# Performance work log

Hardware: AMD Instinct MI355X
Metric: run time of the kernel (lower is better)

Reference implementation:

```python
import jax, jax.numpy as jnp
import numpy as np

N, E, D, H, C = 50000, 800000, 128, 4, 32  # nodes, edges, in/out dim, heads, head dim
NEG_SLOPE = 0.2
LN_EPS = 1e-5
NORM_EPS = 1e-12


def setup_inputs() -> dict:
    key = jax.random.key(0)
    ks = jax.random.split(key, 10)
    s = 1.0 / np.sqrt(D)
    return {
        "x": jax.random.normal(ks[0], (N, D), dtype=jnp.float32),
        "edge_index": jax.random.randint(ks[1], (2, E), 0, N, dtype=jnp.int64),
        "gamma": 1.0 + 0.1 * jax.random.normal(ks[2], (D,), dtype=jnp.float32),
        "beta": 0.1 * jax.random.normal(ks[3], (D,), dtype=jnp.float32),
        "W_l": jax.random.normal(ks[4], (D, H * C), dtype=jnp.float32) * s,
        "b_l": jnp.zeros((H * C,), dtype=jnp.float32),
        "W_r": jax.random.normal(ks[5], (D, H * C), dtype=jnp.float32) * s,
        "b_r": jnp.zeros((H * C,), dtype=jnp.float32),
        "att": jax.random.normal(ks[6], (H, C), dtype=jnp.float32) * s,
        "bias": jnp.zeros((H * C,), dtype=jnp.float32),
        "scale": jnp.array(1.0, dtype=jnp.float32),
    }


def reference(x, edge_index, gamma, beta, W_l, b_l, W_r, b_r, att, bias, scale):
    n = x.shape[0]
    # Pre-activation: LayerNorm -> ReLU (dropout=0 in eval)
    mu = jnp.mean(x, axis=-1, keepdims=True)
    var = jnp.mean(jnp.square(x - mu), axis=-1, keepdims=True)
    h = jax.nn.relu((x - mu) / jnp.sqrt(var + LN_EPS) * gamma + beta)

    # GATv2Conv (PyG defaults: add_self_loops=True, negative_slope=0.2)
    loops = jnp.arange(n, dtype=edge_index.dtype)
    src = jnp.concatenate([edge_index[0], loops])  # message source j
    dst = jnp.concatenate([edge_index[1], loops])  # message target i

    xl = (h @ W_l + b_l).reshape(n, H, C)
    xr = (h @ W_r + b_r).reshape(n, H, C)

    # per-edge GATv2 score: a^T LeakyReLU(xl[j] + xr[i])  -> [E2, H]
    feat = jax.nn.leaky_relu(xl[src] + xr[dst], NEG_SLOPE)
    e = jnp.einsum('ehc,hc->eh', feat, att)

    # segment softmax over incoming edges of each target node
    m = jax.ops.segment_max(e, dst, num_segments=n)
    p = jnp.exp(e - m[dst])
    denom = jax.ops.segment_sum(p, dst, num_segments=n)
    alpha = p / denom[dst]  # [E2, H]

    # scatter-aggregate weighted source features
    msg = alpha[:, :, None] * xl[src]  # [E2, H, C]
    out = jax.ops.segment_sum(msg, dst, num_segments=n).reshape(n, H * C) + bias

    # MsgNorm: normalize(msg) * ||h||_2 * scale
    out_norm = jnp.sqrt(jnp.sum(jnp.square(out), axis=-1, keepdims=True))
    msg_n = out / jnp.maximum(out_norm, NORM_EPS)
    h_norm = jnp.sqrt(jnp.sum(jnp.square(h), axis=-1, keepdims=True))
    gat_out = msg_n * h_norm * scale

    # residual (projection is None since in_channels == out_channels)
    return x + gat_out
```

## Files before the change

### kernel.cpp

```cpp
#include <hip/hip_runtime.h>
#include <hip/hip_bf16.h>
#include <math.h>

#define N_NODES 50000
#define N_EDGES 800000
#define E2 (N_EDGES + N_NODES)
#define D 128

#define NB_LN 12500
#define NB_W 128

#define BSHIFT 8
#define NBUCK 196
#define SCHUNK 4096
#define NB_SC ((E2 + SCHUNK - 1) / SCHUNK)
#define NB_GEMM (((N_NODES + 127) / 128) * 2)

typedef short short8 __attribute__((ext_vector_type(8)));
typedef float f32x4 __attribute__((ext_vector_type(4)));
typedef _Float16 h16x2 __attribute__((ext_vector_type(2)));
typedef _Float16 h16x8 __attribute__((ext_vector_type(8)));

__device__ __forceinline__ float waveReduceSum(float v) {
#pragma unroll
  for (int off = 32; off >= 1; off >>= 1) v += __shfl_xor(v, off);
  return v;
}

__global__ void __launch_bounds__(256) k_pre(
    const float* __restrict__ x, const float* __restrict__ gamma,
    const float* __restrict__ beta, const float* __restrict__ Wl,
    const float* __restrict__ Wr, const int* __restrict__ ei,
    __hip_bfloat16* __restrict__ hb, float* __restrict__ hnorm,
    __hip_bfloat16* __restrict__ Wt, int* __restrict__ bcnt) {
  const int b = blockIdx.x;
  if (b < NB_LN) {
    int wid = threadIdx.x >> 6;
    int lane = threadIdx.x & 63;
    int i = b * 4 + wid;
    const float2 xv = *(const float2*)&x[(size_t)i * D + lane * 2];
    float s = waveReduceSum(xv.x + xv.y);
    float mean = s * (1.0f / D);
    float d0 = xv.x - mean, d1 = xv.y - mean;
    float vs = waveReduceSum(d0 * d0 + d1 * d1);
    float rstd = rsqrtf(vs * (1.0f / D) + 1e-5f);
    const float2 g = *(const float2*)&gamma[lane * 2];
    const float2 bb = *(const float2*)&beta[lane * 2];
    float h0 = fmaxf(d0 * rstd * g.x + bb.x, 0.0f);
    float h1 = fmaxf(d1 * rstd * g.y + bb.y, 0.0f);
    __hip_bfloat162 hv;
    hv.x = __float2bfloat16(h0);
    hv.y = __float2bfloat16(h1);
    *(__hip_bfloat162*)&hb[(size_t)i * D + lane * 2] = hv;
    float ns = waveReduceSum(h0 * h0 + h1 * h1);
    if (lane == 0) hnorm[i] = sqrtf(ns);
  } else if (b < NB_LN + NB_W) {
    int local = b - NB_LN;
    int n = local * 2 + (threadIdx.x >> 7);
    int k = threadIdx.x & 127;
    float v = (n < D) ? Wl[(size_t)k * D + n] : Wr[(size_t)k * D + (n - D)];
    Wt[n * D + k] = __float2bfloat16(v);
  } else {
    __shared__ int c[256];
    const int t = threadIdx.x;
    c[t] = 0;
    __syncthreads();
    const int s0 = (b - NB_LN - NB_W) * SCHUNK;
#pragma unroll
    for (int k = 0; k < 16; ++k) {
      int e = s0 + t + k * 256;
      if (e < E2) {
        int dst = (e < N_EDGES) ? ei[N_EDGES + e] : (e - N_EDGES);
        atomicAdd(&c[dst >> BSHIFT], 1);
      }
    }
    __syncthreads();
    if (c[t]) atomicAdd(&bcnt[t], c[t]);
  }
}

__global__ void __launch_bounds__(256) k_bscatter(const int* __restrict__ ei,
                                                  const int* __restrict__ bcnt,
                                                  int* __restrict__ cnt0,
                                                  int2* __restrict__ bucketed) {
  __shared__ int c[256], base[256], sd[256];
  const int t = threadIdx.x;
  const int own = (t < NBUCK) ? bcnt[t] : 0;
  sd[t] = own;
  c[t] = 0;
  __syncthreads();
  for (int off = 1; off < 256; off <<= 1) {
    int u = 0;
    if (t >= off) u = sd[t - off];
    __syncthreads();
    if (t >= off) sd[t] += u;
    __syncthreads();
  }
  const int boffL = sd[t] - own;
  const int s0 = blockIdx.x * SCHUNK;
#pragma unroll
  for (int k = 0; k < 16; ++k) {
    int e = s0 + t + k * 256;
    if (e < E2) {
      int dst = (e < N_EDGES) ? ei[N_EDGES + e] : (e - N_EDGES);
      atomicAdd(&c[dst >> BSHIFT], 1);
    }
  }
  __syncthreads();
  if (t < NBUCK) {
    base[t] = c[t] ? (boffL + atomicAdd(&cnt0[t], c[t])) : 0;
    c[t] = 0;
  }
  __syncthreads();
#pragma unroll
  for (int k = 0; k < 16; ++k) {
    int e = s0 + t + k * 256;
    if (e < E2) {
      int src, dst;
      if (e < N_EDGES) {
        src = ei[e];
        dst = ei[N_EDGES + e];
      } else {
        src = dst = e - N_EDGES;
      }
      int bk = dst >> BSHIFT;
      int pos = base[bk] + atomicAdd(&c[bk], 1);
      bucketed[pos] = make_int2(src, dst);
    }
  }
}

__global__ void __launch_bounds__(256) k_mid(
    const int2* __restrict__ bucketed, const int* __restrict__ bcnt,
    int* __restrict__ rowptr, int* __restrict__ csr,
    const __hip_bfloat16* __restrict__ hb, const __hip_bfloat16* __restrict__ Wt,
    const float* __restrict__ bL, const float* __restrict__ bR,
    _Float16* __restrict__ xlh, _Float16* __restrict__ xrh) {
  __shared__ char smem[65536];
  const int t = threadIdx.x;
  if (blockIdx.x < NBUCK) {
    int* cnt = (int*)smem;
    int* tsum = cnt + 256;
    int* cursor = tsum + 256;
    int* red = cursor + 256;
    const int b = blockIdx.x;
    const int base = b << BSHIFT;
    const int nnode = min(256, N_NODES - base);
    red[t] = (t < b) ? bcnt[t] : 0;
    cnt[t] = 0;
    __syncthreads();
    for (int off = 128; off >= 1; off >>= 1) {
      if (t < off) red[t] += red[t + off];
      __syncthreads();
    }
    const int e0 = red[0], e1 = red[0] + bcnt[b];
    if (b == 0) {
      if (t == 0) rowptr[N_NODES] = E2;
      if (t < 64) csr[E2 + t] = 0;
    }
    for (int e = e0 + t; e < e1; e += 256) {
      int2 pr = bucketed[e];
      atomicAdd(&cnt[pr.y - base], 1);
    }
    __syncthreads();
    const int own = cnt[t];
    tsum[t] = own;
    __syncthreads();
    for (int off = 1; off < 256; off <<= 1) {
      int u = 0;
      if (t >= off) u = tsum[t - off];
      __syncthreads();
      if (t >= off) tsum[t] += u;
      __syncthreads();
    }
    const int ebase = e0 + tsum[t] - own;
    cursor[t] = ebase;
    if (t < nnode) rowptr[base + t] = ebase;
    __syncthreads();
    for (int e = e0 + t; e < e1; e += 256) {
      int2 pr = bucketed[e];
      int pos = atomicAdd(&cursor[pr.y - base], 1);
      csr[pos] = pr.x;
    }
  } else {
    unsigned short* As = (unsigned short*)smem;
    unsigned short* Bs = As + 128 * 128;
    const int bid = blockIdx.x - NBUCK;
    const int row0 = (bid >> 1) * 128;
    const int nhalf = bid & 1;
    const unsigned short* hu = (const unsigned short*)hb;
    const unsigned short* wu = (const unsigned short*)Wt;
#pragma unroll
    for (int it = 0; it < 8; ++it) {
      int idx = t + it * 256;
      int r = idx >> 4, g = idx & 15;
      int gs = g ^ (r & 15);
      short8 av = {};
      int grow = row0 + r;
      if (grow < N_NODES) av = *(const short8*)&hu[(size_t)grow * D + g * 8];
      *(short8*)&As[r * 128 + gs * 8] = av;
      short8 bv = *(const short8*)&wu[(size_t)(nhalf * 128 + r) * D + g * 8];
      *(short8*)&Bs[r * 128 + gs * 8] = bv;
    }
    __syncthreads();
    const int w = t >> 6, lane = t & 63;
    const int wm = (w >> 1) * 64, wn = (w & 1) * 64;
    const int lr = lane & 15, lq = lane >> 4;
    f32x4 acc[4][4] = {};
#pragma unroll
    for (int kb = 0; kb < 4; ++kb) {
      short8 af[4], bfr[4];
#pragma unroll
      for (int mi = 0; mi < 4; ++mi) {
        int r = wm + mi * 16 + lr;
        int g = (kb * 4 + lq) ^ (r & 15);
        af[mi] = *(const short8*)&As[r * 128 + g * 8];
      }
#pragma unroll
      for (int ni = 0; ni < 4; ++ni) {
        int r = wn + ni * 16 + lr;
        int g = (kb * 4 + lq) ^ (r & 15);
        bfr[ni] = *(const short8*)&Bs[r * 128 + g * 8];
      }
#pragma unroll
      for (int mi = 0; mi < 4; ++mi)
#pragma unroll
        for (int ni = 0; ni < 4; ++ni)
          acc[mi][ni] = __builtin_amdgcn_mfma_f32_16x16x32_bf16(af[mi], bfr[ni],
                                                                acc[mi][ni], 0, 0, 0);
    }
    const float* bb = (nhalf == 0) ? bL : bR;
    _Float16* dst = (nhalf == 0) ? xlh : xrh;
#pragma unroll
    for (int mi = 0; mi < 4; ++mi) {
#pragma unroll
      for (int ni = 0; ni < 4; ++ni) {
#pragma unroll
        for (int r = 0; r < 4; ++r) {
          int row = row0 + wm + mi * 16 + lq * 4 + r;
          int col = wn + ni * 16 + lr;
          if (row < N_NODES)
            dst[(size_t)row * D + col] = (_Float16)(acc[mi][ni][r] + bb[col]);
        }
      }
    }
  }
}

__global__ void __launch_bounds__(256) k_node(
    const float* __restrict__ x, const _Float16* __restrict__ xlh,
    const _Float16* __restrict__ xrh, const float* __restrict__ hnorm,
    const int* __restrict__ rowptr, const int* __restrict__ csr,
    const float* __restrict__ att, const float* __restrict__ bias,
    const float* __restrict__ scale, float* __restrict__ out) {
  const int wid = threadIdx.x >> 6;
  const int lane = threadIdx.x & 63;
  const int g = lane >> 4;
  const int q = lane & 15;
  const int i = blockIdx.x * 16 + wid * 4 + g;

  const h16x8 xrv = *(const h16x8*)(xrh + (size_t)i * D + q * 8);
  h16x2 xr2[4], at2[4];
  {
    const float LOG2E = 1.44269504f;
    const float4 a0 = *(const float4*)&att[q * 8];
    const float4 a1 = *(const float4*)&att[q * 8 + 4];
    at2[0] = (h16x2){(_Float16)(a0.x * LOG2E), (_Float16)(a0.y * LOG2E)};
    at2[1] = (h16x2){(_Float16)(a0.z * LOG2E), (_Float16)(a0.w * LOG2E)};
    at2[2] = (h16x2){(_Float16)(a1.x * LOG2E), (_Float16)(a1.y * LOG2E)};
    at2[3] = (h16x2){(_Float16)(a1.z * LOG2E), (_Float16)(a1.w * LOG2E)};
#pragma unroll
    for (int z = 0; z < 4; ++z) xr2[z] = (h16x2){xrv[2 * z], xrv[2 * z + 1]};
  }
  const h16x2 c02 = {(_Float16)0.2f, (_Float16)0.2f};

  const int e0 = rowptr[i], e1 = rowptr[i + 1];
  const int deg = e1 - e0;
  int maxdeg = deg;
  maxdeg = max(maxdeg, __shfl_xor(maxdeg, 16));
  maxdeg = max(maxdeg, __shfl_xor(maxdeg, 32));

  h16x2 A2[4] = {};
  float S = 0.f;

  int ja = csr[e0];
  h16x8 r0 = *(const h16x8*)(xlh + (size_t)ja * D + q * 8);
  int jb = csr[e0 + 1];
  h16x8 r1 = *(const h16x8*)(xlh + (size_t)jb * D + q * 8);
  int jc = csr[e0 + 2];
  h16x8 r2 = *(const h16x8*)(xlh + (size_t)jc * D + q * 8);
  int jd = csr[e0 + 3];

  for (int it = 0; it < maxdeg; ++it) {
    const h16x8 cur = r0;
    r0 = r1;
    r1 = r2;
    r2 = *(const h16x8*)(xlh + (size_t)jd * D + q * 8);
    jd = csr[e0 + it + 4];
    const bool ok = it < deg;

    h16x2 v2[4];
    v2[0] = (h16x2){cur[0], cur[1]};
    v2[1] = (h16x2){cur[2], cur[3]};
    v2[2] = (h16x2){cur[4], cur[5]};
    v2[3] = (h16x2){cur[6], cur[7]};
    float sc = 0.f;
#pragma unroll
    for (int z = 0; z < 4; ++z) {
      h16x2 f = v2[z] + xr2[z];
      h16x2 lf = __builtin_elementwise_max(f, f * c02);
      sc = __builtin_amdgcn_fdot2(lf, at2[z], sc, false);
    }
    sc += __shfl_xor(sc, 1);
    sc += __shfl_xor(sc, 2);
    const float p = ok ? __builtin_exp2f(sc) : 0.f;
    S += p;
    const _Float16 ph = (_Float16)p;
    const h16x2 p2 = {ph, ph};
#pragma unroll
    for (int z = 0; z < 4; ++z) A2[z] = v2[z] * p2 + A2[z];
  }

  const float si = 1.0f / S;
  float o[8];
  float b8[8];
  *(float4*)&b8[0] = *(const float4*)&bias[q * 8];
  *(float4*)&b8[4] = *(const float4*)&bias[q * 8 + 4];
  float dot = 0.f;
#pragma unroll
  for (int z = 0; z < 4; ++z) {
    o[2 * z] = fmaf((float)A2[z][0], si, b8[2 * z]);
    o[2 * z + 1] = fmaf((float)A2[z][1], si, b8[2 * z + 1]);
    dot = fmaf(o[2 * z], o[2 * z], dot);
    dot = fmaf(o[2 * z + 1], o[2 * z + 1], dot);
  }
#pragma unroll
  for (int off = 8; off >= 1; off >>= 1) dot += __shfl_xor(dot, off, 16);
  const float nrm = sqrtf(dot);
  const float gg = hnorm[i] * scale[0] / fmaxf(nrm, 1e-12f);

  float x8[8];
  *(float4*)&x8[0] = *(const float4*)&x[(size_t)i * D + q * 8];
  *(float4*)&x8[4] = *(const float4*)&x[(size_t)i * D + q * 8 + 4];
  float r8[8];
#pragma unroll
  for (int z = 0; z < 8; ++z) r8[z] = fmaf(o[z], gg, x8[z]);
  *(float4*)&out[(size_t)i * D + q * 8] = *(float4*)&r8[0];
  *(float4*)&out[(size_t)i * D + q * 8 + 4] = *(float4*)&r8[4];
}

extern "C" void kernel_launch(void* const* d_in, const int* in_sizes, int n_in,
                              void* d_out, int out_size, void* d_ws, size_t ws_size,
                              hipStream_t stream) {
  const float* x = (const float*)d_in[0];
  const int* ei = (const int*)d_in[1];
  const float* gamma = (const float*)d_in[2];
  const float* beta = (const float*)d_in[3];
  const float* Wl = (const float*)d_in[4];
  const float* bL = (const float*)d_in[5];
  const float* Wr = (const float*)d_in[6];
  const float* bR = (const float*)d_in[7];
  const float* att = (const float*)d_in[8];
  const float* bias = (const float*)d_in[9];
  const float* scale = (const float*)d_in[10];
  float* out = (float*)d_out;

  int2* bucketed = (int2*)d_ws;
  int* csr = (int*)(bucketed + E2);
  int* rowptr = csr + E2 + 64;
  int* bcnt = rowptr + N_NODES + 16;
  int* cnt0 = bcnt + 256;
  float* hnorm = (float*)(cnt0 + 256);
  __hip_bfloat16* hb = (__hip_bfloat16*)(hnorm + N_NODES);
  __hip_bfloat16* Wt = hb + (size_t)N_NODES * D;
  _Float16* xlh = (_Float16*)(Wt + 256 * D);
  _Float16* xrh = xlh + (size_t)N_NODES * D;

  hipMemsetAsync(bcnt, 0, 512 * sizeof(int), stream);
  k_pre<<<NB_LN + NB_W + NB_SC, 256, 0, stream>>>(x, gamma, beta, Wl, Wr, ei, hb,
                                                  hnorm, Wt, bcnt);
  k_bscatter<<<NB_SC, 256, 0, stream>>>(ei, bcnt, cnt0, bucketed);
  k_mid<<<NBUCK + NB_GEMM, 256, 0, stream>>>(bucketed, bcnt, rowptr, csr, hb, Wt,
                                             bL, bR, xlh, xrh);
  k_node<<<N_NODES / 16, 256, 0, stream>>>(x, xlh, xrh, hnorm, rowptr, csr, att,
                                           bias, scale, out);
}
```

Baseline: 119.9 us.

## Sort nodes by in-degree to balance per-wave edge loops in aggregation

```diff
diff --git a/kernel.cpp b/kernel.cpp
--- a/kernel.cpp
+++ b/kernel.cpp
@@ -14,6 +14,7 @@
 #define NBUCK 196
 #define SCHUNK 4096
 #define NB_SC ((E2 + SCHUNK - 1) / SCHUNK)
+#define NSLICE ((N_NODES + NB_SC - 1) / NB_SC)
 #define NB_GEMM (((N_NODES + 127) / 128) * 2)
 
 typedef short short8 __attribute__((ext_vector_type(8)));
@@ -32,7 +33,8 @@
     const float* __restrict__ beta, const float* __restrict__ Wl,
     const float* __restrict__ Wr, const int* __restrict__ ei,
     __hip_bfloat16* __restrict__ hb, float* __restrict__ hnorm,
-    __hip_bfloat16* __restrict__ Wt, int* __restrict__ bcnt) {
+    __hip_bfloat16* __restrict__ Wt, int* __restrict__ bcnt,
+    int* __restrict__ deg) {
   const int b = blockIdx.x;
   if (b < NB_LN) {
     int wid = threadIdx.x >> 6;
@@ -72,6 +74,7 @@
       if (e < E2) {
         int dst = (e < N_EDGES) ? ei[N_EDGES + e] : (e - N_EDGES);
         atomicAdd(&c[dst >> BSHIFT], 1);
+        atomicAdd(&deg[dst], 1);
       }
     }
     __syncthreads();
@@ -82,12 +85,16 @@
 __global__ void __launch_bounds__(256) k_bscatter(const int* __restrict__ ei,
                                                   const int* __restrict__ bcnt,
                                                   int* __restrict__ cnt0,
-                                                  int2* __restrict__ bucketed) {
+                                                  int2* __restrict__ bucketed,
+                                                  const int* __restrict__ deg,
+                                                  int* __restrict__ hist) {
   __shared__ int c[256], base[256], sd[256];
+  __shared__ int hh[128];
   const int t = threadIdx.x;
   const int own = (t < NBUCK) ? bcnt[t] : 0;
   sd[t] = own;
   c[t] = 0;
+  if (t < 128) hh[t] = 0;
   __syncthreads();
   for (int off = 1; off < 256; off <<= 1) {
     int u = 0;
@@ -128,10 +135,17 @@
       bucketed[pos] = make_int2(src, dst);
     }
   }
+  const int n0 = blockIdx.x * NSLICE;
+  const int n1 = min(n0 + NSLICE, N_NODES);
+  for (int n = n0 + t; n < n1; n += 256) atomicAdd(&hh[min(deg[n], 127)], 1);
+  __syncthreads();
+  if (t < 128 && hh[t]) atomicAdd(&hist[t], hh[t]);
 }
 
 __global__ void __launch_bounds__(256) k_mid(
     const int2* __restrict__ bucketed, const int* __restrict__ bcnt,
+    const int* __restrict__ deg, const int* __restrict__ hist,
+    int* __restrict__ cnt2, int* __restrict__ perm,
     int* __restrict__ rowptr, int* __restrict__ csr,
     const __hip_bfloat16* __restrict__ hb, const __hip_bfloat16* __restrict__ Wt,
     const float* __restrict__ bL, const float* __restrict__ bR,
@@ -139,15 +153,13 @@
   __shared__ char smem[65536];
   const int t = threadIdx.x;
   if (blockIdx.x < NBUCK) {
-    int* cnt = (int*)smem;
-    int* tsum = cnt + 256;
+    int* tsum = (int*)smem;
     int* cursor = tsum + 256;
     int* red = cursor + 256;
     const int b = blockIdx.x;
     const int base = b << BSHIFT;
     const int nnode = min(256, N_NODES - base);
     red[t] = (t < b) ? bcnt[t] : 0;
-    cnt[t] = 0;
     __syncthreads();
     for (int off = 128; off >= 1; off >>= 1) {
       if (t < off) red[t] += red[t + off];
@@ -158,12 +170,7 @@
       if (t == 0) rowptr[N_NODES] = E2;
       if (t < 64) csr[E2 + t] = 0;
     }
-    for (int e = e0 + t; e < e1; e += 256) {
-      int2 pr = bucketed[e];
-      atomicAdd(&cnt[pr.y - base], 1);
-    }
-    __syncthreads();
-    const int own = cnt[t];
+    const int own = (t < nnode) ? deg[base + t] : 0;
     tsum[t] = own;
     __syncthreads();
     for (int off = 1; off < 256; off <<= 1) {
@@ -182,7 +189,7 @@
       int pos = atomicAdd(&cursor[pr.y - base], 1);
       csr[pos] = pr.x;
     }
-  } else {
+  } else if (blockIdx.x < NBUCK + NB_GEMM) {
     unsigned short* As = (unsigned short*)smem;
     unsigned short* Bs = As + 128 * 128;
     const int bid = blockIdx.x - NBUCK;
@@ -244,6 +251,45 @@
         }
       }
     }
+  } else {
+    int* bbase = (int*)smem;
+    int* horig = bbase + 128;
+    int* bc = horig + 128;
+    int* brsv = bc + 128;
+    const int pb = blockIdx.x - NBUCK - NB_GEMM;
+    const int n0 = pb << 8;
+    const int nnode = min(256, N_NODES - n0);
+    if (t < 128) {
+      int hv = hist[t];
+      horig[t] = hv;
+      bbase[t] = hv;
+      bc[t] = 0;
+    }
+    __syncthreads();
+    for (int off = 1; off < 128; off <<= 1) {
+      int u = 0;
+      if (t >= off && t < 128) u = bbase[t - off];
+      __syncthreads();
+      if (t >= off && t < 128) bbase[t] += u;
+      __syncthreads();
+    }
+    if (t < 128) bbase[t] -= horig[t];
+    __syncthreads();
+    int d = 0;
+    if (t < nnode) {
+      d = min(deg[n0 + t], 127);
+      atomicAdd(&bc[d], 1);
+    }
+    __syncthreads();
+    if (t < 128) {
+      brsv[t] = bc[t] ? (bbase[t] + atomicAdd(&cnt2[t], bc[t])) : 0;
+      bc[t] = 0;
+    }
+    __syncthreads();
+    if (t < nnode) {
+      int slot = brsv[d] + atomicAdd(&bc[d], 1);
+      perm[slot] = n0 + t;
+    }
   }
 }
 
@@ -251,13 +297,14 @@
     const float* __restrict__ x, const _Float16* __restrict__ xlh,
     const _Float16* __restrict__ xrh, const float* __restrict__ hnorm,
     const int* __restrict__ rowptr, const int* __restrict__ csr,
-    const float* __restrict__ att, const float* __restrict__ bias,
-    const float* __restrict__ scale, float* __restrict__ out) {
+    const int* __restrict__ perm, const float* __restrict__ att,
+    const float* __restrict__ bias, const float* __restrict__ scale,
+    float* __restrict__ out) {
   const int wid = threadIdx.x >> 6;
   const int lane = threadIdx.x & 63;
   const int g = lane >> 4;
   const int q = lane & 15;
-  const int i = blockIdx.x * 16 + wid * 4 + g;
+  const int i = perm[blockIdx.x * 16 + wid * 4 + g];
 
   const h16x8 xrv = *(const h16x8*)(xrh + (size_t)i * D + q * 8);
   h16x2 xr2[4], at2[4];
@@ -275,8 +322,8 @@
   const h16x2 c02 = {(_Float16)0.2f, (_Float16)0.2f};
 
   const int e0 = rowptr[i], e1 = rowptr[i + 1];
-  const int deg = e1 - e0;
-  int maxdeg = deg;
+  const int deg_ = e1 - e0;
+  int maxdeg = deg_;
   maxdeg = max(maxdeg, __shfl_xor(maxdeg, 16));
   maxdeg = max(maxdeg, __shfl_xor(maxdeg, 32));
 
@@ -297,7 +344,7 @@
     r1 = r2;
     r2 = *(const h16x8*)(xlh + (size_t)jd * D + q * 8);
     jd = csr[e0 + it + 4];
-    const bool ok = it < deg;
+    const bool ok = it < deg_;
 
     h16x2 v2[4];
     v2[0] = (h16x2){cur[0], cur[1]};
@@ -370,18 +417,24 @@
   int* rowptr = csr + E2 + 64;
   int* bcnt = rowptr + N_NODES + 16;
   int* cnt0 = bcnt + 256;
-  float* hnorm = (float*)(cnt0 + 256);
+  int* hist = cnt0 + 256;
+  int* cnt2 = hist + 128;
+  int* deg = cnt2 + 128;
+  int* perm = deg + N_NODES;
+  float* hnorm = (float*)(perm + N_NODES);
   __hip_bfloat16* hb = (__hip_bfloat16*)(hnorm + N_NODES);
   __hip_bfloat16* Wt = hb + (size_t)N_NODES * D;
   _Float16* xlh = (_Float16*)(Wt + 256 * D);
   _Float16* xrh = xlh + (size_t)N_NODES * D;
 
-  hipMemsetAsync(bcnt, 0, 512 * sizeof(int), stream);
+  hipMemsetAsync(bcnt, 0, (size_t)(256 + 256 + 128 + 128 + N_NODES) * sizeof(int),
+                 stream);
   k_pre<<<NB_LN + NB_W + NB_SC, 256, 0, stream>>>(x, gamma, beta, Wl, Wr, ei, hb,
-                                                  hnorm, Wt, bcnt);
-  k_bscatter<<<NB_SC, 256, 0, stream>>>(ei, bcnt, cnt0, bucketed);
-  k_mid<<<NBUCK + NB_GEMM, 256, 0, stream>>>(bucketed, bcnt, rowptr, csr, hb, Wt,
-                                             bL, bR, xlh, xrh);
-  k_node<<<N_NODES / 16, 256, 0, stream>>>(x, xlh, xrh, hnorm, rowptr, csr, att,
-                                           bias, scale, out);
-}
+                                                  hnorm, Wt, bcnt, deg);
+  k_bscatter<<<NB_SC, 256, 0, stream>>>(ei, bcnt, cnt0, bucketed, deg, hist);
+  k_mid<<<NBUCK + NB_GEMM + NBUCK, 256, 0, stream>>>(bucketed, bcnt, deg, hist, cnt2,
+                                                     perm, rowptr, csr, hb, Wt, bL,
+                                                     bR, xlh, xrh);
+  k_node<<<N_NODES / 16, 256, 0, stream>>>(x, xlh, xrh, hnorm, rowptr, csr, perm,
+                                           att, bias, scale, out);
+}
```

New measurement: 153.0 us. 1.28x slower.

## Sort nodes by in-degree within each bucket to balance per-node wavefront work

Applied to the files above, without the earlier changes.

```diff
diff --git a/kernel.cpp b/kernel.cpp
--- a/kernel.cpp
+++ b/kernel.cpp
@@ -132,7 +132,7 @@
 
 __global__ void __launch_bounds__(256) k_mid(
     const int2* __restrict__ bucketed, const int* __restrict__ bcnt,
-    int* __restrict__ rowptr, int* __restrict__ csr,
+    int* __restrict__ rowptr, int* __restrict__ csr, int* __restrict__ perm,
     const __hip_bfloat16* __restrict__ hb, const __hip_bfloat16* __restrict__ Wt,
     const float* __restrict__ bL, const float* __restrict__ bR,
     _Float16* __restrict__ xlh, _Float16* __restrict__ xrh) {
@@ -143,11 +143,15 @@
     int* tsum = cnt + 256;
     int* cursor = tsum + 256;
     int* red = cursor + 256;
+    int* dhist = red + 256;
+    int* dscan = dhist + 128;
+    int* dcur = dscan + 128;
     const int b = blockIdx.x;
     const int base = b << BSHIFT;
     const int nnode = min(256, N_NODES - base);
     red[t] = (t < b) ? bcnt[t] : 0;
     cnt[t] = 0;
+    if (t < 128) dhist[t] = 0;
     __syncthreads();
     for (int off = 128; off >= 1; off >>= 1) {
       if (t < off) red[t] += red[t + off];
@@ -164,6 +168,8 @@
     }
     __syncthreads();
     const int own = cnt[t];
+    const int dbin = min(own, 127);
+    if (t < nnode) atomicAdd(&dhist[dbin], 1);
     tsum[t] = own;
     __syncthreads();
     for (int off = 1; off < 256; off <<= 1) {
@@ -173,10 +179,27 @@
       if (t >= off) tsum[t] += u;
       __syncthreads();
     }
+    if (t < 128) dscan[t] = dhist[t];
+    __syncthreads();
+    for (int off = 1; off < 128; off <<= 1) {
+      int u = 0;
+      if (t >= off && t < 128) u = dscan[t - off];
+      __syncthreads();
+      if (t >= off && t < 128) dscan[t] += u;
+      __syncthreads();
+    }
+    if (t < 128) {
+      dscan[t] -= dhist[t];
+      dcur[t] = 0;
+    }
     const int ebase = e0 + tsum[t] - own;
     cursor[t] = ebase;
     if (t < nnode) rowptr[base + t] = ebase;
     __syncthreads();
+    if (t < nnode) {
+      int slot = dscan[dbin] + atomicAdd(&dcur[dbin], 1);
+      perm[base + slot] = base + t;
+    }
     for (int e = e0 + t; e < e1; e += 256) {
       int2 pr = bucketed[e];
       int pos = atomicAdd(&cursor[pr.y - base], 1);
@@ -251,13 +274,14 @@
     const float* __restrict__ x, const _Float16* __restrict__ xlh,
     const _Float16* __restrict__ xrh, const float* __restrict__ hnorm,
     const int* __restrict__ rowptr, const int* __restrict__ csr,
-    const float* __restrict__ att, const float* __restrict__ bias,
-    const float* __restrict__ scale, float* __restrict__ out) {
+    const int* __restrict__ perm, const float* __restrict__ att,
+    const float* __restrict__ bias, const float* __restrict__ scale,
+    float* __restrict__ out) {
   const int wid = threadIdx.x >> 6;
   const int lane = threadIdx.x & 63;
   const int g = lane >> 4;
   const int q = lane & 15;
-  const int i = blockIdx.x * 16 + wid * 4 + g;
+  const int i = perm[blockIdx.x * 16 + wid * 4 + g];
 
   const h16x8 xrv = *(const h16x8*)(xrh + (size_t)i * D + q * 8);
   h16x2 xr2[4], at2[4];
@@ -370,7 +394,8 @@
   int* rowptr = csr + E2 + 64;
   int* bcnt = rowptr + N_NODES + 16;
   int* cnt0 = bcnt + 256;
-  float* hnorm = (float*)(cnt0 + 256);
+  int* perm = cnt0 + 256;
+  float* hnorm = (float*)(perm + N_NODES);
   __hip_bfloat16* hb = (__hip_bfloat16*)(hnorm + N_NODES);
   __hip_bfloat16* Wt = hb + (size_t)N_NODES * D;
   _Float16* xlh = (_Float16*)(Wt + 256 * D);
@@ -380,8 +405,8 @@
   k_pre<<<NB_LN + NB_W + NB_SC, 256, 0, stream>>>(x, gamma, beta, Wl, Wr, ei, hb,
                                                   hnorm, Wt, bcnt);
   k_bscatter<<<NB_SC, 256, 0, stream>>>(ei, bcnt, cnt0, bucketed);
-  k_mid<<<NBUCK + NB_GEMM, 256, 0, stream>>>(bucketed, bcnt, rowptr, csr, hb, Wt,
-                                             bL, bR, xlh, xrh);
-  k_node<<<N_NODES / 16, 256, 0, stream>>>(x, xlh, xrh, hnorm, rowptr, csr, att,
-                                           bias, scale, out);
-}
+  k_mid<<<NBUCK + NB_GEMM, 256, 0, stream>>>(bucketed, bcnt, rowptr, csr, perm, hb,
+                                             Wt, bL, bR, xlh, xrh);
+  k_node<<<N_NODES / 16, 256, 0, stream>>>(x, xlh, xrh, hnorm, rowptr, csr, perm,
+                                           att, bias, scale, out);
+}
```

New measurement: 134.7 us. 1.12x slower.
